# Kernel optimization log

Hardware: AMD Instinct MI355X
Metric: run time of the kernel (lower is better)

## Reference

```python
import jax, jax.numpy as jnp
import numpy as np
from jax import lax

EPS = 1e-5


def _st_gcn_layer(x, w, b, A):
    # x: (N, C, T, V); w: (K*Co, C, 9, 1); A: (K, V, V) (already scaled by edge importance)
    y = lax.conv_general_dilated(x, w, window_strides=(1, 1),
                                 padding=[(4, 4), (0, 0)],
                                 dimension_numbers=('NCHW', 'OIHW', 'NCHW'))
    y = y + b[None, :, None, None]
    N, KC, T, V = y.shape
    K = A.shape[0]
    y = y.reshape(N, K, KC // K, T, V)
    y = jnp.einsum('nkctv,kvw->nctw', y, A)  # graph convolution
    return jax.nn.relu(y)


def setup_inputs() -> dict:
    key = jax.random.key(0)
    ks = jax.random.split(key, 8)
    N, T, V, C, Co, K, KT = 16, 512, 25, 256, 256, 3, 9
    x = jax.random.normal(ks[0], (N, T, V, C), dtype=jnp.float32)
    bn_gamma = jax.random.uniform(ks[1], (V * C,), dtype=jnp.float32)
    bn_beta = jax.random.normal(ks[2], (V * C,), dtype=jnp.float32)
    bn_mean = jnp.zeros((V * C,), dtype=jnp.float32)
    bn_var = jnp.ones((V * C,), dtype=jnp.float32)
    w_scale = 1.0 / np.sqrt(C * KT)
    w1 = jax.random.normal(ks[3], (K * Co, C, KT, 1), dtype=jnp.float32) * w_scale
    b1 = jax.random.normal(ks[4], (K * Co,), dtype=jnp.float32) * 0.01
    w2 = jax.random.normal(ks[5], (K * Co, Co, KT, 1), dtype=jnp.float32) * w_scale
    b2 = jax.random.normal(ks[6], (K * Co,), dtype=jnp.float32) * 0.01
    ei1 = jnp.ones((K, V, V), dtype=jnp.float32)
    ei2 = jnp.ones((K, V, V), dtype=jnp.float32)
    A = jax.random.uniform(ks[7], (K, V, V), dtype=jnp.float32)
    return {"x": x, "bn_gamma": bn_gamma, "bn_beta": bn_beta, "bn_mean": bn_mean,
            "bn_var": bn_var, "w1": w1, "b1": b1, "ei1": ei1, "w2": w2, "b2": b2,
            "ei2": ei2, "A": A}


def reference(x, bn_gamma, bn_beta, bn_mean, bn_var, w1, b1, ei1, w2, b2, ei2, A):
    N, T, V, C = x.shape
    # data_bn over V*C channels (V-major, C-minor per the torch permutes), eval mode
    xb = jnp.transpose(x, (0, 2, 3, 1)).reshape(N, V * C, T)  # (N, V*C, T)
    inv = bn_gamma / jnp.sqrt(bn_var + EPS)
    xb = (xb - bn_mean[None, :, None]) * inv[None, :, None] + bn_beta[None, :, None]
    xb = jnp.transpose(xb.reshape(N, V, C, T), (0, 2, 3, 1))  # (N, C, T, V)
    h = _st_gcn_layer(xb, w1, b1, A * ei1)
    h = _st_gcn_layer(h, w2, b2, A * ei2)
    return jnp.transpose(h, (0, 2, 3, 1))  # (N, T, V, Cout)
```

## Files before the change

### kernel.cpp

```cpp
#include <hip/hip_runtime.h>
#include <stdint.h>

typedef unsigned short ushortT;
typedef short short8 __attribute__((ext_vector_type(8)));
typedef float f32x4 __attribute__((ext_vector_type(4)));
typedef float f32x2 __attribute__((ext_vector_type(2)));
typedef unsigned short us4 __attribute__((ext_vector_type(4)));

#define TP 520
#define PAD 4
#define XPAD_B 20480
#define ATILE_B 8192

__device__ __forceinline__ unsigned short f2bf(float f) {
  union { float f; unsigned int u; } v; v.f = f;
  unsigned int r = (v.u + 0x7fffu + ((v.u >> 16) & 1u)) >> 16;
  return (unsigned short)r;
}
__device__ __forceinline__ float bf2f(unsigned short b) {
  union { unsigned int u; float f; } v; v.u = ((unsigned int)b) << 16;
  return v.f;
}
__device__ __forceinline__ float ldadp(const void* p, long i, int bf) {
  return bf ? bf2f(((const unsigned short*)p)[i]) : ((const float*)p)[i];
}
__device__ __forceinline__ f32x2 ldadp2(const void* p, long i, int bf) {
  f32x2 r;
  if (bf) {
    unsigned int u = *(const unsigned int*)((const unsigned short*)p + i);
    r[0] = bf2f((unsigned short)(u & 0xffffu));
    r[1] = bf2f((unsigned short)(u >> 16));
  } else {
    r = *(const f32x2*)((const float*)p + i);
  }
  return r;
}

__device__ __forceinline__ void gload16(const void* g, void* l) {
  __builtin_amdgcn_global_load_lds(
      (const __attribute__((address_space(1))) void*)g,
      (__attribute__((address_space(3))) void*)l, 16, 0, 0);
}

__global__ void detect_kernel(const void* var, int* flags) {
  flags[0] = (((const unsigned int*)var)[0] == 0x3F803F80u) ? 1 : 0;
}

__global__ void prep_w_kernel(const void* w, ushortT* __restrict__ Wt, const int* flags) {
  int bf = flags[0];
  long i = (long)blockIdx.x * 256 + threadIdx.x;
  int c = (int)(i & 255);
  long mc = i >> 8;
  int m = (int)(mc % 768);
  int dt = (int)(mc / 768);
  long dst = (((long)(dt * 8 + (c >> 5)) * 768 + m) << 5) + (c & 31);
  Wt[dst] = f2bf(ldadp(w, ((long)m * 256 + c) * 9 + dt, bf));
}

__global__ void prep_ae_kernel(const void* A, const void* ei, const void* b,
                               float* __restrict__ Ae, float* __restrict__ Bsum,
                               const int* flags) {
  __shared__ float ash[1875];
  int bf = flags[0];
  int tid = threadIdx.x;
  for (int i = tid; i < 1875; i += 1024) {
    float ae = ldadp(A, i, bf) * ldadp(ei, i, bf);
    ash[i] = ae; Ae[i] = ae;
  }
  __syncthreads();
  for (int i = tid; i < 6400; i += 1024) {
    int c = i / 25, w = i % 25;
    float s = 0.f;
    for (int k = 0; k < 3; k++) {
      float cs = 0.f;
      for (int v = 0; v < 25; v++) cs += ash[(k * 25 + v) * 25 + w];
      s += ldadp(b, k * 256 + c, bf) * cs;
    }
    Bsum[i] = s;
  }
}

__global__ void pad_kernel(ushortT* __restrict__ Xb) {
  long nv = (long)blockIdx.y * 25 + blockIdx.x;
  int tid = threadIdx.x;
  #pragma unroll
  for (int r = 0; r < 4; r++) {
    Xb[(nv * TP + r) * 256 + tid] = 0;
    Xb[(nv * TP + 516 + r) * 256 + tid] = 0;
  }
}

__global__ void bn_kernel(const void* x, long xoff, const void* gamma, const void* beta,
                          const void* mean, const void* var, const int* flags,
                          ushortT* __restrict__ Xb, long total) {
  long i2 = ((long)blockIdx.x * 256 + threadIdx.x) * 2;
  if (i2 >= total) return;
  int bf = flags[0];
  int c = (int)(i2 & 255);
  long j = i2 >> 8;
  int v = (int)(j % 25); j /= 25;
  int t = (int)(j % 512); j /= 512;
  int nl = (int)j;
  int pc = v * 256 + c;
  f32x2 xv = ldadp2(x, xoff + i2, bf);
  unsigned int outw = 0;
  #pragma unroll
  for (int e = 0; e < 2; e++) {
    float inv = ldadp(gamma, pc + e, bf) * rsqrtf(ldadp(var, pc + e, bf) + 1e-5f);
    float val = (xv[e] - ldadp(mean, pc + e, bf)) * inv + ldadp(beta, pc + e, bf);
    outw |= ((unsigned int)f2bf(val)) << (16 * e);
  }
  *(unsigned int*)(Xb + (((long)(nl * 25 + v)) * TP + t + PAD) * 256 + c) = outw;
}

__global__ __launch_bounds__(256, 2) void conv_kernel(
    const ushortT* __restrict__ Xb, const ushortT* __restrict__ Wt,
    ushortT* __restrict__ Y) {
  __shared__ short8 smem[(2 * XPAD_B + 3 * ATILE_B) / 16];
  char* lds = (char*)smem;
  char* Xl0 = lds;
  char* Xl1 = lds + XPAD_B;
  char* Ap0 = lds + 2 * XPAD_B;
  char* Ap1 = Ap0 + ATILE_B;
  char* Ap2 = Ap0 + 2 * ATILE_B;

  const int tid = threadIdx.x;
  const int lane = tid & 63;
  const int wave = tid >> 6;
  const int wm = wave >> 1, wn = wave & 1;
  const int kb = lane >> 4;
  const int l15 = lane & 15;
  const int wubase = (tid & ~63);

  int bid = blockIdx.x;
  const int v = bid % 25;
  const int rtile = bid / 25;
  const int tt = rtile & 1;
  const int mt = rtile >> 1;
  const int nl = blockIdx.y;
  const int m0 = mt * 128;
  const int t0 = tt * 256;

  const long xrowbase = ((long)(nl * 25 + v)) * TP + t0;

  auto stageX = [&](int cc, char* xb) {
    #pragma unroll
    for (int k = 0; k < 5; k++) {
      int s = k * 256 + tid;
      int r = s >> 2, q = s & 3;
      if (k == 4) r = (r < 264) ? r : 263;
      int ql = q ^ ((r >> 1) & 3);
      gload16(Xb + (xrowbase + r) * 256 + cc * 32 + ql * 8,
              xb + (long)(k * 256 + wubase) * 16);
    }
  };
  auto stageA = [&](int g, char* ab) {
    const ushortT* wb = Wt + (((long)g * 768 + m0) << 5);
    #pragma unroll
    for (int k = 0; k < 2; k++) {
      int s = k * 256 + tid;
      int r = s >> 2, q = s & 3;
      int ql = q ^ ((r >> 1) & 3);
      gload16(wb + (long)(r * 4 + ql) * 8, ab + (long)(k * 256 + wubase) * 16);
    }
  };

  f32x4 acc[4][8];
  #pragma unroll
  for (int i = 0; i < 4; i++)
    #pragma unroll
    for (int j = 0; j < 8; j++) { acc[i][j][0]=0.f; acc[i][j][1]=0.f; acc[i][j][2]=0.f; acc[i][j][3]=0.f; }

  stageX(0, Xl0);
  stageA(0, Ap0);
  stageA(8, Ap1);

  for (int cc = 0; cc < 8; cc++) {
    char* Xcur = (cc & 1) ? Xl1 : Xl0;
    char* Xnext = (cc & 1) ? Xl0 : Xl1;
    #pragma unroll
    for (int dt = 0; dt < 9; dt++) {
      if (dt == 8) { asm volatile("s_waitcnt vmcnt(7)" ::: "memory"); }
      else         { asm volatile("s_waitcnt vmcnt(2)" ::: "memory"); }
      __builtin_amdgcn_s_barrier();

      if (dt <= 6) {
        stageA((dt + 2) * 8 + cc, (dt + 2) % 3 == 0 ? Ap0 : ((dt + 2) % 3 == 1 ? Ap1 : Ap2));
      } else if (dt == 7) {
        stageA(cc + 1, Ap0);
        stageX(cc + 1, Xnext);
      } else {
        stageA(8 + cc + 1, Ap1);
      }

      const char* Acur = (dt % 3 == 0) ? Ap0 : ((dt % 3 == 1) ? Ap1 : Ap2);
      short8 a[4], b[8];
      #pragma unroll
      for (int i = 0; i < 4; i++) {
        int r = wm * 64 + i * 16 + l15;
        int sl = kb ^ ((r >> 1) & 3);
        a[i] = *(const short8*)(Acur + r * 64 + sl * 16);
      }
      #pragma unroll
      for (int j = 0; j < 8; j++) {
        int r = wn * 128 + j * 16 + l15 + dt;
        int sl = kb ^ ((r >> 1) & 3);
        b[j] = *(const short8*)(Xcur + r * 64 + sl * 16);
      }
      #pragma unroll
      for (int i = 0; i < 4; i++)
        #pragma unroll
        for (int j = 0; j < 8; j++)
          acc[i][j] = __builtin_amdgcn_mfma_f32_16x16x32_bf16(a[i], b[j], acc[i][j], 0, 0, 0);
    }
  }

  #pragma unroll
  for (int i = 0; i < 4; i++) {
    #pragma unroll
    for (int j = 0; j < 8; j++) {
      int tg = t0 + wn * 128 + j * 16 + l15;
      int kc = m0 + wm * 64 + i * 16 + (kb << 2);
      long off = (((long)(nl * 512 + tg)) * 25 + v) * 768 + kc;
      us4 u;
      u[0] = f2bf(acc[i][j][0]);
      u[1] = f2bf(acc[i][j][1]);
      u[2] = f2bf(acc[i][j][2]);
      u[3] = f2bf(acc[i][j][3]);
      *(us4*)(Y + off) = u;
    }
  }
}

__global__ __launch_bounds__(256) void gconv_kernel(
    const ushortT* __restrict__ Y, const float* __restrict__ Ae,
    const float* __restrict__ Bsum, ushortT* __restrict__ dstb,
    float* __restrict__ dstf, int mode) {
  __shared__ float aesh[1875];
  const int tid = threadIdx.x;
  const int cp = tid & 127;
  const int c  = cp * 2;
  const int th = tid >> 7;
  const int nl = blockIdx.y;
  const int t0 = blockIdx.x << 2;
  const int tA = t0 + 2 * th;
  for (int i = tid; i < 1875; i += 256) aesh[i] = Ae[i];
  __syncthreads();

  float acc[2][2][25];
  #pragma unroll
  for (int w = 0; w < 25; w++) {
    float b0 = Bsum[c * 25 + w], b1 = Bsum[(c + 1) * 25 + w];
    acc[0][0][w] = b0; acc[0][1][w] = b0;
    acc[1][0][w] = b1; acc[1][1][w] = b1;
  }
  for (int k = 0; k < 3; k++) {
    for (int v = 0; v < 25; v++) {
      long ybase = (((long)(nl * 512 + tA)) * 25 + v) * 768 + k * 256 + c;
      unsigned int ua = *(const unsigned int*)(Y + ybase);
      unsigned int ub = *(const unsigned int*)(Y + ybase + 25L * 768);
      float ya0 = bf2f((unsigned short)(ua & 0xffffu));
      float ya1 = bf2f((unsigned short)(ua >> 16));
      float yb0 = bf2f((unsigned short)(ub & 0xffffu));
      float yb1 = bf2f((unsigned short)(ub >> 16));
      const float* ap = &aesh[(k * 25 + v) * 25];
      #pragma unroll
      for (int w = 0; w < 25; w++) {
        float a = ap[w];
        acc[0][0][w] = fmaf(ya0, a, acc[0][0][w]);
        acc[1][0][w] = fmaf(ya1, a, acc[1][0][w]);
        acc[0][1][w] = fmaf(yb0, a, acc[0][1][w]);
        acc[1][1][w] = fmaf(yb1, a, acc[1][1][w]);
      }
    }
  }
  #pragma unroll
  for (int tt = 0; tt < 2; tt++) {
    int t = tA + tt;
    #pragma unroll
    for (int w = 0; w < 25; w++) {
      float v0 = acc[0][tt][w]; v0 = v0 > 0.f ? v0 : 0.f;
      float v1 = acc[1][tt][w]; v1 = v1 > 0.f ? v1 : 0.f;
      if (mode == 0) {
        unsigned int pk = (unsigned int)f2bf(v0) | ((unsigned int)f2bf(v1) << 16);
        *(unsigned int*)(dstb + (((long)(nl * 25 + w)) * TP + t + PAD) * 256 + c) = pk;
      } else {
        f32x2 pk; pk[0] = v0; pk[1] = v1;
        *(f32x2*)(dstf + (((long)(nl * 512 + t)) * 25 + w) * 256 + c) = pk;
      }
    }
  }
}

extern "C" void kernel_launch(void* const* d_in, const int* in_sizes, int n_in,
                              void* d_out, int out_size, void* d_ws, size_t ws_size,
                              hipStream_t stream) {
  const void* x     = d_in[0];
  const void* gamma = d_in[1];
  const void* beta  = d_in[2];
  const void* mean  = d_in[3];
  const void* var   = d_in[4];
  const void* w1    = d_in[5];
  const void* b1    = d_in[6];
  const void* ei1   = d_in[7];
  const void* w2    = d_in[8];
  const void* b2    = d_in[9];
  const void* ei2   = d_in[10];
  const void* A     = d_in[11];
  float* out = (float*)d_out;

  const size_t WtB  = 9L * 768 * 256 * 2;
  const size_t XbB1 = 25L * TP * 256 * 2;
  const size_t YB1  = 512L * 25 * 768 * 2;
  const size_t fixed = 256 + 2 * WtB + 2 * (1875 * 4) + 2 * (6400 * 4) + 8 * 256;

  int G = 16;
  while (G > 1 && fixed + (size_t)G * (XbB1 + YB1) > ws_size) G >>= 1;

  char* ws = (char*)d_ws;
  size_t off = 0;
  auto alloc = [&](size_t bytes) { char* p = ws + off; off = (off + bytes + 255) & ~(size_t)255; return p; };
  int* flags   = (int*)alloc(256);
  ushortT* Wt1 = (ushortT*)alloc(WtB);
  ushortT* Wt2 = (ushortT*)alloc(WtB);
  float* Ae1   = (float*)alloc(1875 * 4);
  float* Ae2   = (float*)alloc(1875 * 4);
  float* Bs1   = (float*)alloc(6400 * 4);
  float* Bs2   = (float*)alloc(6400 * 4);
  ushortT* Xb  = (ushortT*)alloc((size_t)G * XbB1);
  ushortT* Y   = (ushortT*)alloc((size_t)G * YB1);

  detect_kernel<<<1, 1, 0, stream>>>(var, flags);
  prep_w_kernel<<<6912, 256, 0, stream>>>(w1, Wt1, flags);
  prep_w_kernel<<<6912, 256, 0, stream>>>(w2, Wt2, flags);
  prep_ae_kernel<<<1, 1024, 0, stream>>>(A, ei1, b1, Ae1, Bs1, flags);
  prep_ae_kernel<<<1, 1024, 0, stream>>>(A, ei2, b2, Ae2, Bs2, flags);

  for (int n0 = 0; n0 < 16; n0 += G) {
    long xoff = (long)n0 * 512 * 25 * 256;
    float* out_c = out + (size_t)n0 * 512 * 25 * 256;
    long total = (long)G * 512 * 25 * 256;

    pad_kernel<<<dim3(25, G), 256, 0, stream>>>(Xb);
    bn_kernel<<<(int)((total / 2 + 255) / 256), 256, 0, stream>>>(x, xoff, gamma, beta, mean, var, flags, Xb, total);

    conv_kernel<<<dim3(300, G), 256, 0, stream>>>(Xb, Wt1, Y);
    gconv_kernel<<<dim3(128, G), 256, 0, stream>>>(Y, Ae1, Bs1, Xb, (float*)nullptr, 0);
    conv_kernel<<<dim3(300, G), 256, 0, stream>>>(Xb, Wt2, Y);
    gconv_kernel<<<dim3(128, G), 256, 0, stream>>>(Y, Ae2, Bs2, (ushortT*)nullptr, out_c, 1);
  }
}
```

Before: 1.694 ms.

## Load conv weight fragments directly into registers, drop LDS weight staging

Weight (A) tiles now go straight from global memory into per-wave register fragments with a register double buffer, instead of being staged through three LDS buffers. The per-tap barriers and vmcnt waits are replaced by one full wait and barrier per channel chunk, which cuts LDS footprint and synchronisation. The costs are uncoalesced 16-byte global weight loads repeated by each wave, more register pressure, and a full vmcnt(0) drain each chunk that can expose load latency.

```diff
diff --git a/kernel.cpp b/kernel.cpp
--- a/kernel.cpp
+++ b/kernel.cpp
@@ -10,7 +10,6 @@
 #define TP 520
 #define PAD 4
 #define XPAD_B 20480
-#define ATILE_B 8192
 
 __device__ __forceinline__ unsigned short f2bf(float f) {
   union { float f; unsigned int u; } v; v.f = f;
@@ -116,13 +115,10 @@
 __global__ __launch_bounds__(256, 2) void conv_kernel(
     const ushortT* __restrict__ Xb, const ushortT* __restrict__ Wt,
     ushortT* __restrict__ Y) {
-  __shared__ short8 smem[(2 * XPAD_B + 3 * ATILE_B) / 16];
+  __shared__ short8 smem[2 * XPAD_B / 16];
   char* lds = (char*)smem;
-  char* Xl0 = lds;
-  char* Xl1 = lds + XPAD_B;
-  char* Ap0 = lds + 2 * XPAD_B;
-  char* Ap1 = Ap0 + ATILE_B;
-  char* Ap2 = Ap0 + 2 * ATILE_B;
+  char* Xbuf0 = lds;
+  char* Xbuf1 = lds + XPAD_B;
 
   const int tid = threadIdx.x;
   const int lane = tid & 63;
@@ -154,15 +150,11 @@
               xb + (long)(k * 256 + wubase) * 16);
     }
   };
-  auto stageA = [&](int g, char* ab) {
-    const ushortT* wb = Wt + (((long)g * 768 + m0) << 5);
-    #pragma unroll
-    for (int k = 0; k < 2; k++) {
-      int s = k * 256 + tid;
-      int r = s >> 2, q = s & 3;
-      int ql = q ^ ((r >> 1) & 3);
-      gload16(wb + (long)(r * 4 + ql) * 8, ab + (long)(k * 256 + wubase) * 16);
-    }
+  auto loadA = [&](int g, short8* dst) {
+    const ushortT* wb = Wt + (((long)g * 768 + m0 + wm * 64 + l15) << 5) + kb * 8;
+    #pragma unroll
+    for (int i = 0; i < 4; i++)
+      dst[i] = *(const short8*)(wb + ((long)i * 16 << 5));
   };
 
   f32x4 acc[4][8];
@@ -171,36 +163,27 @@
     #pragma unroll
     for (int j = 0; j < 8; j++) { acc[i][j][0]=0.f; acc[i][j][1]=0.f; acc[i][j][2]=0.f; acc[i][j][3]=0.f; }
 
-  stageX(0, Xl0);
-  stageA(0, Ap0);
-  stageA(8, Ap1);
+  short8 aA[4], aB[4];
+
+  stageX(0, Xbuf0);
+  loadA(0, aA);
 
   for (int cc = 0; cc < 8; cc++) {
-    char* Xcur = (cc & 1) ? Xl1 : Xl0;
-    char* Xnext = (cc & 1) ? Xl0 : Xl1;
+    char* Xcur = (cc & 1) ? Xbuf1 : Xbuf0;
+    asm volatile("s_waitcnt vmcnt(0) lgkmcnt(0)" ::: "memory");
+    __builtin_amdgcn_s_barrier();
+    __builtin_amdgcn_sched_barrier(0);
+    if (cc < 7) stageX(cc + 1, (cc & 1) ? Xbuf0 : Xbuf1);
+
     #pragma unroll
     for (int dt = 0; dt < 9; dt++) {
-      if (dt == 8) { asm volatile("s_waitcnt vmcnt(7)" ::: "memory"); }
-      else         { asm volatile("s_waitcnt vmcnt(2)" ::: "memory"); }
-      __builtin_amdgcn_s_barrier();
-
-      if (dt <= 6) {
-        stageA((dt + 2) * 8 + cc, (dt + 2) % 3 == 0 ? Ap0 : ((dt + 2) % 3 == 1 ? Ap1 : Ap2));
-      } else if (dt == 7) {
-        stageA(cc + 1, Ap0);
-        stageX(cc + 1, Xnext);
-      } else {
-        stageA(8 + cc + 1, Ap1);
-      }
-
-      const char* Acur = (dt % 3 == 0) ? Ap0 : ((dt % 3 == 1) ? Ap1 : Ap2);
-      short8 a[4], b[8];
-      #pragma unroll
-      for (int i = 0; i < 4; i++) {
-        int r = wm * 64 + i * 16 + l15;
-        int sl = kb ^ ((r >> 1) & 3);
-        a[i] = *(const short8*)(Acur + r * 64 + sl * 16);
-      }
+      const int par = (cc + dt) & 1;
+      short8* acur = par ? aB : aA;
+      short8* anxt = par ? aA : aB;
+      int gn = (dt == 8) ? ((cc < 7) ? (cc + 1) : 0) : ((dt + 1) * 8 + cc);
+      loadA(gn, anxt);
+
+      short8 b[8];
       #pragma unroll
       for (int j = 0; j < 8; j++) {
         int r = wn * 128 + j * 16 + l15 + dt;
@@ -211,7 +194,7 @@
       for (int i = 0; i < 4; i++)
         #pragma unroll
         for (int j = 0; j < 8; j++)
-          acc[i][j] = __builtin_amdgcn_mfma_f32_16x16x32_bf16(a[i], b[j], acc[i][j], 0, 0, 0);
+          acc[i][j] = __builtin_amdgcn_mfma_f32_16x16x32_bf16(acur[i], b[j], acc[i][j], 0, 0, 0);
     }
   }
 
```

After: 3.341 ms. +97.2%, slower.
